# Performance work log

Hardware: AMD Instinct MI355X
Metric: run time of the kernel (lower is better)

Reference implementation:

```python
import jax, jax.numpy as jnp
import numpy as np

N_NODES = 50000


def setup_inputs() -> dict:
    key = jax.random.key(0)
    k1, k2, k3, k4, k5 = jax.random.split(key, 5)
    h = jax.random.normal(k1, (50000, 256), dtype=jnp.float32)
    norm = jax.random.uniform(k2, (50000, 1), dtype=jnp.float32)
    weight = jax.random.normal(k3, (256, 96), dtype=jnp.float32) * (1.0 / np.sqrt(96.0))
    src = jax.random.randint(k4, (800000,), 0, N_NODES, dtype=jnp.int64)
    dst = jax.random.randint(k5, (800000,), 0, N_NODES, dtype=jnp.int64)
    return {"h": h, "norm": norm, "weight": weight, "src": src, "dst": dst}


def reference(h, norm, weight, src, dst):
    # dense projection: [N, in] @ [in, out] -> [N, out]
    hw = jnp.matmul(h, weight)
    # pre-aggregation degree norm
    hw = hw * norm
    # copy_src + sum: gather messages from src, scatter-add into dst
    msgs = hw[src]  # [E, out]
    agg = jax.ops.segment_sum(msgs, dst, num_segments=N_NODES)
    # post-aggregation degree norm + activation
    out = jax.nn.relu(agg * norm)
    return out
```

## Files before the change

### kernel.cpp

```cpp
#include <hip/hip_runtime.h>

#define M_NODES 50000
#define KDIM    256
#define NDIM    96
#define NEDGE   800000
#define BM      64
#define GEMM_BLKS 782
#define NPB     64
#define NBUCK   782
#define CAPB    1536
#define EPB     2048
#define NBLK_SC 391
#define TOT_BLKS (GEMM_BLKS + NBLK_SC)

typedef short bf16x8 __attribute__((ext_vector_type(8)));
typedef float f32x4  __attribute__((ext_vector_type(4)));

__device__ inline unsigned short f2bf(float x) {
    unsigned u = __float_as_uint(x);
    u = (u + 0x7fffu + ((u >> 16) & 1u)) >> 16;
    return (unsigned short)u;
}
__device__ inline unsigned pack2bf(float x, float y) {
    return (unsigned)f2bf(x) | ((unsigned)f2bf(y) << 16);
}

__global__ __launch_bounds__(256) void prep_w_kernel(
    const float* __restrict__ w, unsigned short* __restrict__ wt,
    int* __restrict__ gcursor)
{
    const int b = blockIdx.x, t = threadIdx.x;
    if (b < 96) {
        wt[b * 256 + t] = f2bf(w[(size_t)t * NDIM + b]);
    } else {
        for (int i = t; i < NBUCK; i += 256) gcursor[i] = i * CAPB;
    }
}

__global__ __launch_bounds__(256) void fused_gemm_scatter_kernel(
    const float* __restrict__ h, const float* __restrict__ norm,
    const unsigned short* __restrict__ wt, unsigned short* __restrict__ hwb,
    const int* __restrict__ src, const int* __restrict__ dst,
    int* __restrict__ gcursor, unsigned* __restrict__ binned)
{
    __shared__ __align__(16) char smem[32768];

    const int tid = threadIdx.x;
    const unsigned bx = blockIdx.x;

    if (bx % 3 != 2) {
        const int gid = (int)bx - (int)((bx + 1) / 3);
        char* a_lds = smem;
        const int lane = tid & 63;
        const int wv   = tid >> 6;
        const int row0 = gid * BM;

#pragma unroll
        for (int it = 0; it < 8; ++it) {
            int idx = tid + it * 256;
            int r   = idx >> 5;
            int u   = idx & 31;
            int row = row0 + r;
            if (row >= M_NODES) row = M_NODES - 1;
            const float* hp = h + (size_t)row * KDIM + u * 8;
            float4 p = *reinterpret_cast<const float4*>(hp);
            float4 q = *reinterpret_cast<const float4*>(hp + 4);
            uint4 o;
            o.x = pack2bf(p.x, p.y); o.y = pack2bf(p.z, p.w);
            o.z = pack2bf(q.x, q.y); o.w = pack2bf(q.z, q.w);
            *reinterpret_cast<uint4*>(a_lds + r * 512 + ((u * 16) ^ ((r & 7) << 4))) = o;
        }
        __syncthreads();

        f32x4 acc[6];
#pragma unroll
        for (int f = 0; f < 6; ++f) acc[f] = (f32x4){0.f, 0.f, 0.f, 0.f};

        const int ar = wv * 16 + (lane & 15);
        const int kg = lane >> 4;
        const unsigned short* __restrict__ wb =
            wt + (size_t)(lane & 15) * KDIM + kg * 8;

#pragma unroll
        for (int s = 0; s < 8; ++s) {
            const int kb = s * 64 + kg * 16;
            bf16x8 a = *reinterpret_cast<const bf16x8*>(
                a_lds + ar * 512 + (kb ^ ((ar & 7) << 4)));
#pragma unroll
            for (int f = 0; f < 6; ++f) {
                bf16x8 b = *reinterpret_cast<const bf16x8*>(
                    wb + (size_t)f * 16 * KDIM + s * 32);
                acc[f] = __builtin_amdgcn_mfma_f32_16x16x32_bf16(a, b, acc[f], 0, 0, 0);
            }
        }

        const int crow = wv * 16 + (lane >> 4) * 4;
        const int ccol = lane & 15;
#pragma unroll
        for (int r = 0; r < 4; ++r) {
            int row = row0 + crow + r;
            if (row < M_NODES) {
                float nv = norm[row];
#pragma unroll
                for (int f = 0; f < 6; ++f)
                    hwb[(size_t)row * NDIM + f * 16 + ccol] = f2bf(acc[f][r] * nv);
            }
        }
    } else {
        int* s_cnt  = reinterpret_cast<int*>(smem);
        int* s_base = s_cnt + NBUCK;
        const int blk = (int)(bx / 3);
        const int e0 = blk * EPB;
        const int e1 = (e0 + EPB < NEDGE) ? e0 + EPB : NEDGE;

        for (int i = tid; i < NBUCK; i += 256) s_cnt[i] = 0;
        __syncthreads();
        for (int e = e0 + tid; e < e1; e += 256)
            atomicAdd(&s_cnt[dst[e] >> 6], 1);
        __syncthreads();
        for (int i = tid; i < NBUCK; i += 256) {
            int c = s_cnt[i];
            s_base[i] = c ? atomicAdd(&gcursor[i], c) : 0;
        }
        __syncthreads();
        for (int i = tid; i < NBUCK; i += 256) s_cnt[i] = 0;
        __syncthreads();
        for (int e = e0 + tid; e < e1; e += 256) {
            int d = dst[e];
            int b = d >> 6;
            int pos = s_base[b] + atomicAdd(&s_cnt[b], 1);
            if (pos < (b + 1) * CAPB)
                binned[pos] = ((unsigned)(d & 63) << 16) | (unsigned)src[e];
        }
    }
}

#define ACCV(A, v)                                     \
    A[0] += __uint_as_float((v).x << 16);              \
    A[1] += __uint_as_float((v).x & 0xffff0000u);      \
    A[2] += __uint_as_float((v).y << 16);              \
    A[3] += __uint_as_float((v).y & 0xffff0000u);      \
    A[4] += __uint_as_float((v).z << 16);              \
    A[5] += __uint_as_float((v).z & 0xffff0000u);      \
    A[6] += __uint_as_float((v).w << 16);              \
    A[7] += __uint_as_float((v).w & 0xffff0000u);

__global__ __launch_bounds__(256) void csr_agg_kernel(
    const unsigned* __restrict__ binned, const int* __restrict__ gcursor,
    const unsigned short* __restrict__ hwb, const float* __restrict__ norm,
    float* __restrict__ out)
{
    __shared__ unsigned eL[CAPB];
    __shared__ unsigned short oL[CAPB];
    __shared__ int cnt[NPB];
    __shared__ int pfxE[NPB];

    const int b  = blockIdx.x;
    const int t  = threadIdx.x;
    const int e0 = b * CAPB;
    int cntE = gcursor[b] - e0;
    if (cntE > CAPB) cntE = CAPB;

    for (int i = t; i < cntE; i += 256) eL[i] = binned[e0 + i];
    if (t < NPB) cnt[t] = 0;
    __syncthreads();
    for (int i = t; i < cntE; i += 256)
        atomicAdd(&cnt[(eL[i] >> 16) & 63], 1);
    __syncthreads();
    if (t < NPB) {
        int v = cnt[t];
        int x = v;
#pragma unroll
        for (int st = 1; st < 64; st <<= 1) {
            int o = __shfl_up(x, st, 64);
            if (t >= st) x += o;
        }
        int ex = x - v;
        pfxE[t] = ex;
        cnt[t]  = ex;
    }
    __syncthreads();
    for (int i = t; i < cntE; i += 256) {
        unsigned v = eL[i];
        int d = (v >> 16) & 63;
        int p = atomicAdd(&cnt[d], 1);
        oL[p] = (unsigned short)(v & 0xffffu);
    }
    __syncthreads();

#pragma unroll
    for (int pass = 0; pass < 3; ++pass) {
        const int u     = pass * 256 + t;
        const int node  = u / 12;
        const int c8    = u - node * 12;
        const int gnode = b * NPB + node;
        if (gnode < M_NODES) {
            const int s0 = pfxE[node];
            const int s1 = cnt[node];
            float acc[8]  = {0.f, 0.f, 0.f, 0.f, 0.f, 0.f, 0.f, 0.f};
            float acc2[8] = {0.f, 0.f, 0.f, 0.f, 0.f, 0.f, 0.f, 0.f};
            int e = s0;
            for (; e + 4 <= s1; e += 4) {
                int a0 = oL[e], a1 = oL[e + 1], a2 = oL[e + 2], a3 = oL[e + 3];
                uint4 v0 = *reinterpret_cast<const uint4*>(hwb + (size_t)a0 * NDIM + c8 * 8);
                uint4 v1 = *reinterpret_cast<const uint4*>(hwb + (size_t)a1 * NDIM + c8 * 8);
                uint4 v2 = *reinterpret_cast<const uint4*>(hwb + (size_t)a2 * NDIM + c8 * 8);
                uint4 v3 = *reinterpret_cast<const uint4*>(hwb + (size_t)a3 * NDIM + c8 * 8);
                ACCV(acc, v0); ACCV(acc2, v1); ACCV(acc, v2); ACCV(acc2, v3);
            }
            for (; e < s1; ++e) {
                int a0 = oL[e];
                uint4 v0 = *reinterpret_cast<const uint4*>(hwb + (size_t)a0 * NDIM + c8 * 8);
                ACCV(acc, v0);
            }
            const float nv = norm[gnode];
            float4 o0, o1;
            o0.x = fmaxf((acc[0] + acc2[0]) * nv, 0.f);
            o0.y = fmaxf((acc[1] + acc2[1]) * nv, 0.f);
            o0.z = fmaxf((acc[2] + acc2[2]) * nv, 0.f);
            o0.w = fmaxf((acc[3] + acc2[3]) * nv, 0.f);
            o1.x = fmaxf((acc[4] + acc2[4]) * nv, 0.f);
            o1.y = fmaxf((acc[5] + acc2[5]) * nv, 0.f);
            o1.z = fmaxf((acc[6] + acc2[6]) * nv, 0.f);
            o1.w = fmaxf((acc[7] + acc2[7]) * nv, 0.f);
            float4* po = reinterpret_cast<float4*>(out + (size_t)gnode * NDIM + c8 * 8);
            po[0] = o0; po[1] = o1;
        }
    }
}

extern "C" void kernel_launch(void* const* d_in, const int* in_sizes, int n_in,
                              void* d_out, int out_size, void* d_ws, size_t ws_size,
                              hipStream_t stream)
{
    const float* h    = (const float*)d_in[0];
    const float* norm = (const float*)d_in[1];
    const float* w    = (const float*)d_in[2];
    const int*   src  = (const int*)d_in[3];
    const int*   dst  = (const int*)d_in[4];
    float* out = (float*)d_out;

    unsigned short* hwb = (unsigned short*)d_ws;
    unsigned short* wt  = hwb + (size_t)M_NODES * NDIM;
    int* gcursor = (int*)(wt + KDIM * NDIM);
    unsigned* binned = (unsigned*)(gcursor + 800);

    prep_w_kernel<<<97, 256, 0, stream>>>(w, wt, gcursor);
    fused_gemm_scatter_kernel<<<TOT_BLKS, 256, 0, stream>>>(
        h, norm, wt, hwb, src, dst, gcursor, binned);
    csr_agg_kernel<<<NBUCK, 256, 0, stream>>>(binned, gcursor, hwb, norm, out);
}
```

Measured before the change: 74.79 us.

## Split fused GEMM/scatter kernel, stage weights in LDS, widen aggregation blocks

```diff
diff --git a/kernel.cpp b/kernel.cpp
--- a/kernel.cpp
+++ b/kernel.cpp
@@ -11,7 +11,6 @@
 #define CAPB    1536
 #define EPB     2048
 #define NBLK_SC 391
-#define TOT_BLKS (GEMM_BLKS + NBLK_SC)
 
 typedef short bf16x8 __attribute__((ext_vector_type(8)));
 typedef float f32x4  __attribute__((ext_vector_type(4)));
@@ -37,101 +36,108 @@
     }
 }
 
-__global__ __launch_bounds__(256) void fused_gemm_scatter_kernel(
+__global__ __launch_bounds__(256) void gemm_mfma_kernel(
     const float* __restrict__ h, const float* __restrict__ norm,
-    const unsigned short* __restrict__ wt, unsigned short* __restrict__ hwb,
+    const unsigned short* __restrict__ wt, unsigned short* __restrict__ hwb)
+{
+    __shared__ __align__(16) char smem[81920];
+
+    const int tid = threadIdx.x;
+    char* w_lds = smem;
+    char* a_lds = smem + 49152;
+    const int lane = tid & 63;
+    const int wv   = tid >> 6;
+    const int row0 = blockIdx.x * BM;
+
+#pragma unroll
+    for (int it = 0; it < 8; ++it) {
+        int idx = tid + it * 256;
+        int r   = idx >> 5;
+        int u   = idx & 31;
+        int row = row0 + r;
+        if (row >= M_NODES) row = M_NODES - 1;
+        const float* hp = h + (size_t)row * KDIM + u * 8;
+        float4 p = *reinterpret_cast<const float4*>(hp);
+        float4 q = *reinterpret_cast<const float4*>(hp + 4);
+        uint4 o;
+        o.x = pack2bf(p.x, p.y); o.y = pack2bf(p.z, p.w);
+        o.z = pack2bf(q.x, q.y); o.w = pack2bf(q.z, q.w);
+        *reinterpret_cast<uint4*>(a_lds + r * 512 + ((u * 16) ^ ((r & 7) << 4))) = o;
+    }
+#pragma unroll
+    for (int it = 0; it < 12; ++it) {
+        int idx = tid + it * 256;
+        int n   = idx >> 5;
+        int kb  = (idx & 31) * 16;
+        uint4 v = *reinterpret_cast<const uint4*>(
+            reinterpret_cast<const char*>(wt) + n * 512 + kb);
+        *reinterpret_cast<uint4*>(w_lds + n * 512 + (kb ^ ((n & 7) << 4))) = v;
+    }
+    __syncthreads();
+
+    f32x4 acc[6];
+#pragma unroll
+    for (int f = 0; f < 6; ++f) acc[f] = (f32x4){0.f, 0.f, 0.f, 0.f};
+
+    const int ar = wv * 16 + (lane & 15);
+    const int kg = lane >> 4;
+
+#pragma unroll
+    for (int s = 0; s < 8; ++s) {
+        const int kb = s * 64 + kg * 16;
+        bf16x8 a = *reinterpret_cast<const bf16x8*>(
+            a_lds + ar * 512 + (kb ^ ((ar & 7) << 4)));
+#pragma unroll
+        for (int f = 0; f < 6; ++f) {
+            int n = f * 16 + (lane & 15);
+            bf16x8 b = *reinterpret_cast<const bf16x8*>(
+                w_lds + n * 512 + (kb ^ ((n & 7) << 4)));
+            acc[f] = __builtin_amdgcn_mfma_f32_16x16x32_bf16(a, b, acc[f], 0, 0, 0);
+        }
+    }
+
+    const int crow = wv * 16 + (lane >> 4) * 4;
+    const int ccol = lane & 15;
+#pragma unroll
+    for (int r = 0; r < 4; ++r) {
+        int row = row0 + crow + r;
+        if (row < M_NODES) {
+            float nv = norm[row];
+#pragma unroll
+            for (int f = 0; f < 6; ++f)
+                hwb[(size_t)row * NDIM + f * 16 + ccol] = f2bf(acc[f][r] * nv);
+        }
+    }
+}
+
+__global__ __launch_bounds__(256) void bin_scatter_kernel(
     const int* __restrict__ src, const int* __restrict__ dst,
     int* __restrict__ gcursor, unsigned* __restrict__ binned)
 {
-    __shared__ __align__(16) char smem[32768];
-
+    __shared__ int s_cnt[NBUCK];
+    __shared__ int s_base[NBUCK];
     const int tid = threadIdx.x;
-    const unsigned bx = blockIdx.x;
-
-    if (bx % 3 != 2) {
-        const int gid = (int)bx - (int)((bx + 1) / 3);
-        char* a_lds = smem;
-        const int lane = tid & 63;
-        const int wv   = tid >> 6;
-        const int row0 = gid * BM;
-
-#pragma unroll
-        for (int it = 0; it < 8; ++it) {
-            int idx = tid + it * 256;
-            int r   = idx >> 5;
-            int u   = idx & 31;
-            int row = row0 + r;
-            if (row >= M_NODES) row = M_NODES - 1;
-            const float* hp = h + (size_t)row * KDIM + u * 8;
-            float4 p = *reinterpret_cast<const float4*>(hp);
-            float4 q = *reinterpret_cast<const float4*>(hp + 4);
-            uint4 o;
-            o.x = pack2bf(p.x, p.y); o.y = pack2bf(p.z, p.w);
-            o.z = pack2bf(q.x, q.y); o.w = pack2bf(q.z, q.w);
-            *reinterpret_cast<uint4*>(a_lds + r * 512 + ((u * 16) ^ ((r & 7) << 4))) = o;
-        }
-        __syncthreads();
-
-        f32x4 acc[6];
-#pragma unroll
-        for (int f = 0; f < 6; ++f) acc[f] = (f32x4){0.f, 0.f, 0.f, 0.f};
-
-        const int ar = wv * 16 + (lane & 15);
-        const int kg = lane >> 4;
-        const unsigned short* __restrict__ wb =
-            wt + (size_t)(lane & 15) * KDIM + kg * 8;
-
-#pragma unroll
-        for (int s = 0; s < 8; ++s) {
-            const int kb = s * 64 + kg * 16;
-            bf16x8 a = *reinterpret_cast<const bf16x8*>(
-                a_lds + ar * 512 + (kb ^ ((ar & 7) << 4)));
-#pragma unroll
-            for (int f = 0; f < 6; ++f) {
-                bf16x8 b = *reinterpret_cast<const bf16x8*>(
-                    wb + (size_t)f * 16 * KDIM + s * 32);
-                acc[f] = __builtin_amdgcn_mfma_f32_16x16x32_bf16(a, b, acc[f], 0, 0, 0);
-            }
-        }
-
-        const int crow = wv * 16 + (lane >> 4) * 4;
-        const int ccol = lane & 15;
-#pragma unroll
-        for (int r = 0; r < 4; ++r) {
-            int row = row0 + crow + r;
-            if (row < M_NODES) {
-                float nv = norm[row];
-#pragma unroll
-                for (int f = 0; f < 6; ++f)
-                    hwb[(size_t)row * NDIM + f * 16 + ccol] = f2bf(acc[f][r] * nv);
-            }
-        }
-    } else {
-        int* s_cnt  = reinterpret_cast<int*>(smem);
-        int* s_base = s_cnt + NBUCK;
-        const int blk = (int)(bx / 3);
-        const int e0 = blk * EPB;
-        const int e1 = (e0 + EPB < NEDGE) ? e0 + EPB : NEDGE;
-
-        for (int i = tid; i < NBUCK; i += 256) s_cnt[i] = 0;
-        __syncthreads();
-        for (int e = e0 + tid; e < e1; e += 256)
-            atomicAdd(&s_cnt[dst[e] >> 6], 1);
-        __syncthreads();
-        for (int i = tid; i < NBUCK; i += 256) {
-            int c = s_cnt[i];
-            s_base[i] = c ? atomicAdd(&gcursor[i], c) : 0;
-        }
-        __syncthreads();
-        for (int i = tid; i < NBUCK; i += 256) s_cnt[i] = 0;
-        __syncthreads();
-        for (int e = e0 + tid; e < e1; e += 256) {
-            int d = dst[e];
-            int b = d >> 6;
-            int pos = s_base[b] + atomicAdd(&s_cnt[b], 1);
-            if (pos < (b + 1) * CAPB)
-                binned[pos] = ((unsigned)(d & 63) << 16) | (unsigned)src[e];
-        }
+    const int e0 = blockIdx.x * EPB;
+    const int e1 = (e0 + EPB < NEDGE) ? e0 + EPB : NEDGE;
+
+    for (int i = tid; i < NBUCK; i += 256) s_cnt[i] = 0;
+    __syncthreads();
+    for (int e = e0 + tid; e < e1; e += 256)
+        atomicAdd(&s_cnt[dst[e] >> 6], 1);
+    __syncthreads();
+    for (int i = tid; i < NBUCK; i += 256) {
+        int c = s_cnt[i];
+        s_base[i] = c ? atomicAdd(&gcursor[i], c) : 0;
+    }
+    __syncthreads();
+    for (int i = tid; i < NBUCK; i += 256) s_cnt[i] = 0;
+    __syncthreads();
+    for (int e = e0 + tid; e < e1; e += 256) {
+        int d = dst[e];
+        int b = d >> 6;
+        int pos = s_base[b] + atomicAdd(&s_cnt[b], 1);
+        if (pos < (b + 1) * CAPB)
+            binned[pos] = ((unsigned)(d & 63) << 16) | (unsigned)src[e];
     }
 }
 
@@ -145,7 +151,7 @@
     A[6] += __uint_as_float((v).w << 16);              \
     A[7] += __uint_as_float((v).w & 0xffff0000u);
 
-__global__ __launch_bounds__(256) void csr_agg_kernel(
+__global__ __launch_bounds__(768) void csr_agg_kernel(
     const unsigned* __restrict__ binned, const int* __restrict__ gcursor,
     const unsigned short* __restrict__ hwb, const float* __restrict__ norm,
     float* __restrict__ out)
@@ -161,10 +167,10 @@
     int cntE = gcursor[b] - e0;
     if (cntE > CAPB) cntE = CAPB;
 
-    for (int i = t; i < cntE; i += 256) eL[i] = binned[e0 + i];
+    for (int i = t; i < cntE; i += 768) eL[i] = binned[e0 + i];
     if (t < NPB) cnt[t] = 0;
     __syncthreads();
-    for (int i = t; i < cntE; i += 256)
+    for (int i = t; i < cntE; i += 768)
         atomicAdd(&cnt[(eL[i] >> 16) & 63], 1);
     __syncthreads();
     if (t < NPB) {
@@ -180,7 +186,7 @@
         cnt[t]  = ex;
     }
     __syncthreads();
-    for (int i = t; i < cntE; i += 256) {
+    for (int i = t; i < cntE; i += 768) {
         unsigned v = eL[i];
         int d = (v >> 16) & 63;
         int p = atomicAdd(&cnt[d], 1);
@@ -188,44 +194,40 @@
     }
     __syncthreads();
 
-#pragma unroll
-    for (int pass = 0; pass < 3; ++pass) {
-        const int u     = pass * 256 + t;
-        const int node  = u / 12;
-        const int c8    = u - node * 12;
-        const int gnode = b * NPB + node;
-        if (gnode < M_NODES) {
-            const int s0 = pfxE[node];
-            const int s1 = cnt[node];
-            float acc[8]  = {0.f, 0.f, 0.f, 0.f, 0.f, 0.f, 0.f, 0.f};
-            float acc2[8] = {0.f, 0.f, 0.f, 0.f, 0.f, 0.f, 0.f, 0.f};
-            int e = s0;
-            for (; e + 4 <= s1; e += 4) {
-                int a0 = oL[e], a1 = oL[e + 1], a2 = oL[e + 2], a3 = oL[e + 3];
-                uint4 v0 = *reinterpret_cast<const uint4*>(hwb + (size_t)a0 * NDIM + c8 * 8);
-                uint4 v1 = *reinterpret_cast<const uint4*>(hwb + (size_t)a1 * NDIM + c8 * 8);
-                uint4 v2 = *reinterpret_cast<const uint4*>(hwb + (size_t)a2 * NDIM + c8 * 8);
-                uint4 v3 = *reinterpret_cast<const uint4*>(hwb + (size_t)a3 * NDIM + c8 * 8);
-                ACCV(acc, v0); ACCV(acc2, v1); ACCV(acc, v2); ACCV(acc2, v3);
-            }
-            for (; e < s1; ++e) {
-                int a0 = oL[e];
-                uint4 v0 = *reinterpret_cast<const uint4*>(hwb + (size_t)a0 * NDIM + c8 * 8);
-                ACCV(acc, v0);
-            }
-            const float nv = norm[gnode];
-            float4 o0, o1;
-            o0.x = fmaxf((acc[0] + acc2[0]) * nv, 0.f);
-            o0.y = fmaxf((acc[1] + acc2[1]) * nv, 0.f);
-            o0.z = fmaxf((acc[2] + acc2[2]) * nv, 0.f);
-            o0.w = fmaxf((acc[3] + acc2[3]) * nv, 0.f);
-            o1.x = fmaxf((acc[4] + acc2[4]) * nv, 0.f);
-            o1.y = fmaxf((acc[5] + acc2[5]) * nv, 0.f);
-            o1.z = fmaxf((acc[6] + acc2[6]) * nv, 0.f);
-            o1.w = fmaxf((acc[7] + acc2[7]) * nv, 0.f);
-            float4* po = reinterpret_cast<float4*>(out + (size_t)gnode * NDIM + c8 * 8);
-            po[0] = o0; po[1] = o1;
-        }
+    const int node  = t / 12;
+    const int c8    = t - node * 12;
+    const int gnode = b * NPB + node;
+    if (gnode < M_NODES) {
+        const int s0 = pfxE[node];
+        const int s1 = cnt[node];
+        float acc[8]  = {0.f, 0.f, 0.f, 0.f, 0.f, 0.f, 0.f, 0.f};
+        float acc2[8] = {0.f, 0.f, 0.f, 0.f, 0.f, 0.f, 0.f, 0.f};
+        int e = s0;
+        for (; e + 4 <= s1; e += 4) {
+            int a0 = oL[e], a1 = oL[e + 1], a2 = oL[e + 2], a3 = oL[e + 3];
+            uint4 v0 = *reinterpret_cast<const uint4*>(hwb + (size_t)a0 * NDIM + c8 * 8);
+            uint4 v1 = *reinterpret_cast<const uint4*>(hwb + (size_t)a1 * NDIM + c8 * 8);
+            uint4 v2 = *reinterpret_cast<const uint4*>(hwb + (size_t)a2 * NDIM + c8 * 8);
+            uint4 v3 = *reinterpret_cast<const uint4*>(hwb + (size_t)a3 * NDIM + c8 * 8);
+            ACCV(acc, v0); ACCV(acc2, v1); ACCV(acc, v2); ACCV(acc2, v3);
+        }
+        for (; e < s1; ++e) {
+            int a0 = oL[e];
+            uint4 v0 = *reinterpret_cast<const uint4*>(hwb + (size_t)a0 * NDIM + c8 * 8);
+            ACCV(acc, v0);
+        }
+        const float nv = norm[gnode];
+        float4 o0, o1;
+        o0.x = fmaxf((acc[0] + acc2[0]) * nv, 0.f);
+        o0.y = fmaxf((acc[1] + acc2[1]) * nv, 0.f);
+        o0.z = fmaxf((acc[2] + acc2[2]) * nv, 0.f);
+        o0.w = fmaxf((acc[3] + acc2[3]) * nv, 0.f);
+        o1.x = fmaxf((acc[4] + acc2[4]) * nv, 0.f);
+        o1.y = fmaxf((acc[5] + acc2[5]) * nv, 0.f);
+        o1.z = fmaxf((acc[6] + acc2[6]) * nv, 0.f);
+        o1.w = fmaxf((acc[7] + acc2[7]) * nv, 0.f);
+        float4* po = reinterpret_cast<float4*>(out + (size_t)gnode * NDIM + c8 * 8);
+        po[0] = o0; po[1] = o1;
     }
 }
 
@@ -246,7 +248,7 @@
     unsigned* binned = (unsigned*)(gcursor + 800);
 
     prep_w_kernel<<<97, 256, 0, stream>>>(w, wt, gcursor);
-    fused_gemm_scatter_kernel<<<TOT_BLKS, 256, 0, stream>>>(
-        h, norm, wt, hwb, src, dst, gcursor, binned);
-    csr_agg_kernel<<<NBUCK, 256, 0, stream>>>(binned, gcursor, hwb, norm, out);
-}
+    bin_scatter_kernel<<<NBLK_SC, 256, 0, stream>>>(src, dst, gcursor, binned);
+    gemm_mfma_kernel<<<GEMM_BLKS, 256, 0, stream>>>(h, norm, wt, hwb);
+    csr_agg_kernel<<<NBUCK, 768, 0, stream>>>(binned, gcursor, hwb, norm, out);
+}
```

After: 73.19 us. 1.02x faster.
